# Kernel optimization log

Hardware: AMD Instinct MI355X
Metric: run time of the kernel (lower is better)

## Reference

```python
import jax, jax.numpy as jnp
import numpy as np
import math

HID, HEADS, HD = 1024, 16, 64
DFF = 4 * HID
EPS = 1e-6
RES_SCALE = 0.5

def build_alibi_slopes(n_heads):
    def get_slopes(power):
        start = 2 ** (-2 ** (-(math.log2(power) - 3)))
        return [start * start ** i for i in range(power)]
    if math.log2(n_heads).is_integer():
        slopes = get_slopes(n_heads)
    else:
        closest = 2 ** math.floor(math.log2(n_heads))
        slopes = get_slopes(closest)
        extra = get_slopes(2 * closest)
        slopes = slopes + extra[0::2][: n_heads - closest]
    return jnp.asarray(np.array(slopes, dtype=np.float32))

def rmsnorm(x, w):
    var = jnp.mean(x * x, axis=-1, keepdims=True)
    return x * jax.lax.rsqrt(var + EPS) * w

def setup_inputs() -> dict:
    key = jax.random.key(0)
    ks = jax.random.split(key, 12)
    s = lambda d: 1.0 / math.sqrt(d)
    return {
        "x": jax.random.normal(ks[0], (2, 2048, HID), dtype=jnp.float32),
        "norm1_w": jnp.ones((HID,), jnp.float32),
        "Wq": jax.random.normal(ks[1], (HID, HEADS * HD), jnp.float32) * s(HID),
        "bq": jax.random.normal(ks[2], (HEADS * HD,), jnp.float32) * 0.01,
        "Wk": jax.random.normal(ks[3], (HID, HEADS * HD), jnp.float32) * s(HID),
        "bk": jax.random.normal(ks[4], (HEADS * HD,), jnp.float32) * 0.01,
        "Wv": jax.random.normal(ks[5], (HID, HEADS * HD), jnp.float32) * s(HID),
        "Wo": jax.random.normal(ks[6], (HEADS * HD, HID), jnp.float32) * s(HEADS * HD),
        "norm2_w": jnp.ones((HID,), jnp.float32),
        "W1": jax.random.normal(ks[7], (HID, DFF), jnp.float32) * s(HID),
        "b1": jax.random.normal(ks[8], (DFF,), jnp.float32) * 0.01,
        "W2": jax.random.normal(ks[9], (DFF, HID), jnp.float32) * s(DFF),
        "b2": jax.random.normal(ks[10], (HID,), jnp.float32) * 0.01,
    }

def reference(x, norm1_w, Wq, bq, Wk, bk, Wv, Wo, norm2_w, W1, b1, W2, b2):
    b, s, _ = x.shape
    scale = HD ** -0.5
    xn = rmsnorm(x, norm1_w)
    q = (xn @ Wq + bq).reshape(b, s, HEADS, HD).transpose(0, 2, 1, 3)
    k = (xn @ Wk + bk).reshape(b, s, HEADS, HD).transpose(0, 2, 1, 3)
    v = (xn @ Wv).reshape(b, s, HEADS, HD).transpose(0, 2, 1, 3)
    scores = jnp.einsum('bhqd,bhkd->bhqk', q, k) * scale
    pos = jnp.arange(s)
    dist = jnp.abs(pos[None, :] - pos[:, None]).astype(scores.dtype)  # [s,s]
    slopes = build_alibi_slopes(HEADS)
    bias = -slopes[:, None, None] * dist[None, :, :]  # [h,s,s]
    scores = scores + bias[None]
    weights = jax.nn.softmax(scores, axis=-1)
    attn = jnp.einsum('bhqk,bhkd->bhqd', weights, v)
    attn = attn.transpose(0, 2, 1, 3).reshape(b, s, HEADS * HD)
    x = x + attn @ Wo
    xn2 = rmsnorm(x, norm2_w)
    h = jax.nn.gelu(xn2 @ W1 + b1, approximate=False)
    x = x + RES_SCALE * (h @ W2 + b2)
    return x
```

## Files before the change

kernel.cpp:

```cpp
#include <hip/hip_runtime.h>
#include <hip/hip_bf16.h>
#include <math.h>

#define S_LEN   2048
#define HIDN    1024
#define NHEADS  16
#define HDIM    64
#define NTOK    4096
#define DFFN    4096

#define LOG2E 1.44269504088896f

typedef __attribute__((ext_vector_type(8))) __bf16 bf16x8;
typedef __attribute__((ext_vector_type(4))) float  f32x4;

static __device__ __forceinline__ ushort f2bf(float f) {
  union { float f; unsigned u; } v; v.f = f;
  unsigned u = v.u;
  unsigned r = (u + 0x7fffu + ((u >> 16) & 1u)) >> 16;
  return (ushort)r;
}

#define GLOAD16(gp, lp)                                                              \
  __builtin_amdgcn_global_load_lds((const __attribute__((address_space(1))) void*)(gp), \
                                   (__attribute__((address_space(3))) void*)(lp), 16, 0, 0)

__global__ __launch_bounds__(256) void convert_all(const float* __restrict__ Wq,
                                                   const float* __restrict__ Wk,
                                                   const float* __restrict__ Wv,
                                                   const float* __restrict__ Wo,
                                                   const float* __restrict__ W1,
                                                   const float* __restrict__ W2,
                                                   ushort* __restrict__ wqkvT,
                                                   ushort* __restrict__ woT,
                                                   ushort* __restrict__ w1T,
                                                   ushort* __restrict__ w2T) {
  __shared__ float tile[32][33];
  int id = blockIdx.x;
  const float* W; ushort* WT; int K, N, tl;
  if (id < 3072) {
    int i = id >> 10; tl = id & 1023;
    W = (i == 0) ? Wq : (i == 1) ? Wk : Wv;
    WT = wqkvT + i * 1024 * 1024; K = 1024; N = 1024;
  } else if (id < 4096) { tl = id - 3072; W = Wo; WT = woT; K = 1024; N = 1024; }
  else if (id < 8192)   { tl = id - 4096; W = W1; WT = w1T; K = 1024; N = 4096; }
  else                  { tl = id - 8192; W = W2; WT = w2T; K = 4096; N = 1024; }
  int ntn = N >> 5;
  int n0 = (tl % ntn) * 32, k0 = (tl / ntn) * 32;
  int tx = threadIdx.x & 31, ty = threadIdx.x >> 5;
#pragma unroll
  for (int i = 0; i < 4; i++)
    tile[ty + i * 8][tx] = W[(size_t)(k0 + ty + i * 8) * N + n0 + tx];
  __syncthreads();
#pragma unroll
  for (int i = 0; i < 4; i++)
    WT[(size_t)(n0 + ty + i * 8) * K + k0 + tx] = f2bf(tile[tx][ty + i * 8]);
}

__global__ __launch_bounds__(256) void rmsnorm_kernel(const float* __restrict__ x,
                                                      const float* __restrict__ w,
                                                      ushort* __restrict__ out) {
  int row = blockIdx.x, t = threadIdx.x;
  const float4* x4 = (const float4*)(x + (size_t)row * HIDN);
  float4 v = x4[t];
  float ss = v.x * v.x + v.y * v.y + v.z * v.z + v.w * v.w;
#pragma unroll
  for (int m = 32; m; m >>= 1) ss += __shfl_xor(ss, m, 64);
  __shared__ float wsum[4];
  if ((t & 63) == 0) wsum[t >> 6] = ss;
  __syncthreads();
  float tot = wsum[0] + wsum[1] + wsum[2] + wsum[3];
  float rs = rsqrtf(tot * (1.0f / HIDN) + 1e-6f);
  const float4* w4 = (const float4*)w;
  float4 wv = w4[t];
  ushort4 o;
  o.x = f2bf(v.x * rs * wv.x);
  o.y = f2bf(v.y * rs * wv.y);
  o.z = f2bf(v.z * rs * wv.z);
  o.w = f2bf(v.w * rs * wv.w);
  *(ushort4*)(out + (size_t)row * HIDN + t * 4) = o;
}

template <int EPI, int TM>
__global__ __launch_bounds__(256, 3) void gemm_bt(const ushort* __restrict__ A,
                                                  const ushort* __restrict__ B,
                                                  int M, int N, int K,
                                                  const float* __restrict__ bias,
                                                  const float* __restrict__ resid,
                                                  float* __restrict__ outf,
                                                  ushort* __restrict__ outb,
                                                  ushort* __restrict__ qb,
                                                  ushort* __restrict__ kb,
                                                  ushort* __restrict__ vb) {
  constexpr int NF = (TM == 128) ? 4 : 2;
  __shared__ __align__(16) ushort As[TM * 64];
  __shared__ __align__(16) ushort Bs[128 * 64];
  int t = threadIdx.x;
  int w = t >> 6, l = t & 63;
  int wmr = (TM == 128) ? (w >> 1) * 64 : 0;
  int wnc = (TM == 128) ? (w & 1) * 64 : w * 32;
  int lr = l & 15, lg = l >> 4;

  int nwg = gridDim.x * gridDim.y;
  int bid = blockIdx.y * gridDim.x + blockIdx.x;
  int swz = (bid & 7) * (nwg >> 3) + (bid >> 3);
  int bx = swz % gridDim.x, by = swz / gridDim.x;
  int m0 = bx * TM, n0 = by * 128;

  int srl = l >> 3;
  int sg  = ((l & 7) ^ srl) * 8;
  const ushort* Ag = A + (size_t)(m0 + w * (TM / 4) + srl) * K + sg;
  const ushort* Bg = B + (size_t)(n0 + w * 32 + srl) * K + sg;
  ushort* Asw = &As[(w * (TM / 4)) * 64];
  ushort* Bsw = &Bs[(w * 32) * 64];

  f32x4 acc[4][NF] = {};

  for (int k0 = 0; k0 < K; k0 += 64) {
#pragma unroll
    for (int c = 0; c < TM / 32; c++)
      GLOAD16(Ag + (size_t)(8 * c) * K + k0, Asw + (8 * c) * 64);
#pragma unroll
    for (int c = 0; c < 4; c++)
      GLOAD16(Bg + (size_t)(8 * c) * K + k0, Bsw + (8 * c) * 64);
    __syncthreads();

    bf16x8 af[4][2], bfr[NF][2];
#pragma unroll
    for (int mf = 0; mf < 4; mf++)
#pragma unroll
      for (int ks = 0; ks < 2; ks++)
        af[mf][ks] = *(const bf16x8*)(&As[(wmr + mf * 16 + lr) * 64 +
                                          (((ks * 4 + lg) ^ (lr & 7)) << 3)]);
#pragma unroll
    for (int nf = 0; nf < NF; nf++)
#pragma unroll
      for (int ks = 0; ks < 2; ks++)
        bfr[nf][ks] = *(const bf16x8*)(&Bs[(wnc + nf * 16 + lr) * 64 +
                                           (((ks * 4 + lg) ^ (lr & 7)) << 3)]);
#pragma unroll
    for (int mf = 0; mf < 4; mf++)
#pragma unroll
      for (int nf = 0; nf < NF; nf++) {
        acc[mf][nf] = __builtin_amdgcn_mfma_f32_16x16x32_bf16(af[mf][0], bfr[nf][0], acc[mf][nf], 0, 0, 0);
        acc[mf][nf] = __builtin_amdgcn_mfma_f32_16x16x32_bf16(af[mf][1], bfr[nf][1], acc[mf][nf], 0, 0, 0);
      }
    __syncthreads();
  }

  int lg4 = lg * 4;
  if constexpr (EPI == 0) {
#pragma unroll
    for (int mf = 0; mf < 4; mf++) {
      int row0 = m0 + wmr + mf * 16 + lg4;
      int bb = row0 >> 11, ss0 = row0 & 2047;
#pragma unroll
      for (int nf = 0; nf < NF; nf++) {
        int col = n0 + wnc + nf * 16 + lr;
        int which = col >> 10, nn = col & 1023;
        int hh = nn >> 6, dd = nn & 63;
        float bcol = (which == 0) ? bias[nn] : (which == 1) ? resid[nn] : 0.0f;
        if (which == 2) {
          ushort4 o;
          o.x = f2bf(acc[mf][nf][0]);
          o.y = f2bf(acc[mf][nf][1]);
          o.z = f2bf(acc[mf][nf][2]);
          o.w = f2bf(acc[mf][nf][3]);
          *(ushort4*)(vb + ((size_t)(bb * NHEADS + hh) * HDIM + dd) * S_LEN + ss0) = o;
        } else {
#pragma unroll
          for (int r = 0; r < 4; r++) {
            float v = acc[mf][nf][r] + bcol;
            size_t idx = ((size_t)(bb * NHEADS + hh) * S_LEN + ss0 + r) * HDIM + dd;
            if (which == 0) qb[idx] = f2bf(v * (0.125f * LOG2E));
            else kb[idx] = f2bf(v);
          }
        }
      }
    }
  } else {
#pragma unroll
    for (int mf = 0; mf < 4; mf++) {
#pragma unroll
      for (int nf = 0; nf < NF; nf++) {
#pragma unroll
        for (int r = 0; r < 4; r++) {
          int row = m0 + wmr + mf * 16 + lg4 + r;
          int col = n0 + wnc + nf * 16 + lr;
          float v = acc[mf][nf][r];
          if constexpr (EPI == 1) {
            outf[(size_t)row * HIDN + col] = resid[(size_t)row * HIDN + col] + v;
          } else if constexpr (EPI == 2) {
            float tv = v + bias[col];
            float gl = 0.5f * tv * (1.0f + erff(tv * 0.70710678118f));
            outb[(size_t)row * DFFN + col] = f2bf(gl);
          } else {
            outf[(size_t)row * HIDN + col] =
                resid[(size_t)row * HIDN + col] + 0.5f * (v + bias[col]);
          }
        }
      }
    }
  }
}

__global__ __launch_bounds__(256, 4) void attn_kernel(const ushort* __restrict__ qb,
                                                      const ushort* __restrict__ kb,
                                                      const ushort* __restrict__ vt,
                                                      ushort* __restrict__ attn_out) {
  __shared__ __align__(16) ushort Ks[2][64 * 64];
  __shared__ __align__(16) ushort VTs[2][64 * 64];
  int t = threadIdx.x;
  int w = t >> 6, l = t & 63;
  int lr = l & 15, lg = l >> 4, g8 = lg * 8;

  int nwg = gridDim.x;
  int bid = blockIdx.x;
  int blk = (bid & 7) * (nwg >> 3) + (bid >> 3);
  int qt = blk & 31;
  int bh = blk >> 5;
  int h = bh & 15;
  float slope2 = exp2f(-0.5f * (float)(h + 1)) * LOG2E;
  float s64v = slope2 * 64.0f;
  int q0 = qt * 64;
  const ushort* qp = qb + (size_t)bh * S_LEN * HDIM;
  const ushort* kp = kb + (size_t)bh * S_LEN * HDIM;
  const ushort* vp = vt + (size_t)bh * HDIM * S_LEN;

  int S0 = (l >> 3) & 3;
  size_t kof0 = (size_t)(w * 16 + (l >> 3)) * HDIM + (size_t)(((l & 7) ^ S0) * 8);
  size_t kof1 = (size_t)(w * 16 + 8 + (l >> 3)) * HDIM + (size_t)(((l & 7) ^ S0 ^ 4) * 8);
  size_t vof0 = (size_t)(w * 16 + (l >> 3)) * S_LEN + (size_t)(((l & 7) ^ S0) * 8);
  size_t vof1 = (size_t)(w * 16 + 8 + (l >> 3)) * S_LEN + (size_t)(((l & 7) ^ S0 ^ 4) * 8);

  auto stage = [&](int tile, int b) {
    const ushort* ks_ = kp + (size_t)tile * 64 * HDIM;
    const ushort* vs_ = vp + tile * 64;
    GLOAD16(ks_ + kof0, &Ks[b][(w * 16) * 64]);
    GLOAD16(ks_ + kof1, &Ks[b][(w * 16 + 8) * 64]);
    GLOAD16(vs_ + vof0, &VTs[b][(w * 16) * 64]);
    GLOAD16(vs_ + vof1, &VTs[b][(w * 16 + 8) * 64]);
  };

  bf16x8 qf[2];
#pragma unroll
  for (int ks = 0; ks < 2; ks++)
    qf[ks] = *(const bf16x8*)(qp + (size_t)(q0 + w * 16 + lr) * HDIM + ks * 32 + g8);

  f32x4 ao[4] = {};
  float mrow = -INFINITY, lden = 0.f;

  int qabs = q0 + w * 16 + lr;
  f32x4 biasv[4];
  if (qt > 0) {
#pragma unroll
    for (int nf = 0; nf < 4; nf++)
#pragma unroll
      for (int r = 0; r < 4; r++)
        biasv[nf][r] = -slope2 * (float)(qabs - (32 * (nf >> 1) + 8 * lg + 4 * (nf & 1) + r));
  }

  int kbase_row = ((lr >> 2) << 3) + (lr & 3);
  int SK = (lr & 3) | (((lr >> 2) & 1) << 2);
  int SV = (lr & 3) | (((lr >> 3) & 1) << 2);

  stage(0, 0);
  __syncthreads();

  for (int tt = 0; tt < S_LEN / 64; tt++) {
    int cur = tt & 1;
    if (tt + 1 < S_LEN / 64) stage(tt + 1, cur ^ 1);
    bool diag = (tt == qt);

    f32x4 sc[4];
    __builtin_amdgcn_s_setprio(1);
#pragma unroll
    for (int nf = 0; nf < 4; nf++) {
      int kvr = kbase_row + ((nf & 1) << 2) + ((nf >> 1) << 5);
      f32x4 a = diag ? f32x4{0.f, 0.f, 0.f, 0.f} : biasv[nf];
#pragma unroll
      for (int ks = 0; ks < 2; ks++) {
        bf16x8 kf = *(const bf16x8*)(&Ks[cur][kvr * 64 + (((ks * 4 + lg) ^ SK) << 3)]);
        a = __builtin_amdgcn_mfma_f32_16x16x32_bf16(kf, qf[ks], a, 0, 0, 0);
      }
      sc[nf] = a;
    }
    __builtin_amdgcn_s_setprio(0);

    if (diag) {
      int qq = w * 16 + lr;
#pragma unroll
      for (int nf = 0; nf < 4; nf++)
#pragma unroll
        for (int r = 0; r < 4; r++) {
          int kvloc = 32 * (nf >> 1) + 8 * lg + 4 * (nf & 1) + r;
          sc[nf][r] -= slope2 * fabsf((float)(qq - kvloc));
          biasv[nf][r] = -slope2 * (float)(64 + kvloc - qq);
        }
    }

    float mx = -INFINITY;
#pragma unroll
    for (int nf = 0; nf < 4; nf++)
#pragma unroll
      for (int r = 0; r < 4; r++) mx = fmaxf(mx, sc[nf][r]);
    mx = fmaxf(mx, __shfl_xor(mx, 16, 64));
    mx = fmaxf(mx, __shfl_xor(mx, 32, 64));

    if (__any(mx > mrow)) {
      float mn = fmaxf(mrow, mx);
      float scl = exp2f(mrow - mn);
      mrow = mn;
      lden *= scl;
      float so[4];
#pragma unroll
      for (int r = 0; r < 4; r++) so[r] = __shfl(scl, lg * 4 + r, 64);
#pragma unroll
      for (int nf = 0; nf < 4; nf++)
#pragma unroll
        for (int r = 0; r < 4; r++) ao[nf][r] *= so[r];
    }

    float su = 0.f;
#pragma unroll
    for (int nf = 0; nf < 4; nf++)
#pragma unroll
      for (int r = 0; r < 4; r++) {
        float p = exp2f(sc[nf][r] - mrow);
        sc[nf][r] = p;
        su += p;
      }
    su += __shfl_xor(su, 16, 64);
    su += __shfl_xor(su, 32, 64);
    lden += su;

    bf16x8 pf[2];
#pragma unroll
    for (int ks = 0; ks < 2; ks++)
#pragma unroll
      for (int j = 0; j < 8; j++)
        pf[ks][j] = (__bf16)sc[2 * ks + (j >> 2)][j & 3];

    __builtin_amdgcn_s_setprio(1);
#pragma unroll
    for (int nf = 0; nf < 4; nf++) {
      int d = nf * 16 + lr;
#pragma unroll
      for (int ks = 0; ks < 2; ks++) {
        bf16x8 vf = *(const bf16x8*)(&VTs[cur][d * 64 + (((ks * 4 + lg) ^ SV) << 3)]);
        ao[nf] = __builtin_amdgcn_mfma_f32_16x16x32_bf16(pf[ks], vf, ao[nf], 0, 0, 0);
      }
    }
    __builtin_amdgcn_s_setprio(0);

    int next = tt + 1;
    if (!diag && next != qt) {
      float dd = (next < qt) ? s64v : -s64v;
#pragma unroll
      for (int nf = 0; nf < 4; nf++)
#pragma unroll
        for (int r = 0; r < 4; r++) biasv[nf][r] += dd;
    }
    __syncthreads();
  }

  float inv[4];
#pragma unroll
  for (int r = 0; r < 4; r++) inv[r] = 1.0f / __shfl(lden, lg * 4 + r, 64);
  int token_base = (bh >> 4) * S_LEN + q0 + w * 16;
#pragma unroll
  for (int nf = 0; nf < 4; nf++) {
#pragma unroll
    for (int r = 0; r < 4; r++) {
      int token = token_base + lg * 4 + r;
      int d = nf * 16 + lr;
      attn_out[(size_t)token * HIDN + h * HDIM + d] = f2bf(ao[nf][r] * inv[r]);
    }
  }
}

extern "C" void kernel_launch(void* const* d_in, const int* in_sizes, int n_in,
                              void* d_out, int out_size, void* d_ws, size_t ws_size,
                              hipStream_t stream) {
  const float* x   = (const float*)d_in[0];
  const float* n1w = (const float*)d_in[1];
  const float* Wq  = (const float*)d_in[2];
  const float* bq  = (const float*)d_in[3];
  const float* Wk  = (const float*)d_in[4];
  const float* bk  = (const float*)d_in[5];
  const float* Wv  = (const float*)d_in[6];
  const float* Wo  = (const float*)d_in[7];
  const float* n2w = (const float*)d_in[8];
  const float* W1  = (const float*)d_in[9];
  const float* b1  = (const float*)d_in[10];
  const float* W2  = (const float*)d_in[11];
  const float* b2  = (const float*)d_in[12];
  float* out = (float*)d_out;

  char* ws = (char*)d_ws;
  ushort* xn     = (ushort*)(ws + 0);
  ushort* wqkvT  = (ushort*)(ws + 8388608);
  ushort* woT    = (ushort*)(ws + 14680064);
  ushort* w1T    = (ushort*)(ws + 16777216);
  ushort* w2T    = (ushort*)(ws + 25165824);
  ushort* qbuf   = (ushort*)(ws + 33566720);
  ushort* kbuf   = (ushort*)(ws + 41955328);
  ushort* vtbuf  = (ushort*)(ws + 50343936);
  ushort* attnb  = (ushort*)(ws + 58732544);
  float*  x2     = (float*)(ws + 67121152);
  ushort* xn2    = (ushort*)(ws + 83898368);
  ushort* hbuf   = qbuf;

  dim3 blk(256);

  convert_all<<<dim3(12288), blk, 0, stream>>>(Wq, Wk, Wv, Wo, W1, W2,
                                               wqkvT, woT, w1T, w2T);
  rmsnorm_kernel<<<NTOK, blk, 0, stream>>>(x, n1w, xn);
  gemm_bt<0, 128><<<dim3(32, 24), blk, 0, stream>>>(xn, wqkvT, NTOK, 3 * HIDN, HIDN,
                                                    bq, bk, nullptr, nullptr,
                                                    qbuf, kbuf, vtbuf);
  attn_kernel<<<dim3(32 * 32), blk, 0, stream>>>(qbuf, kbuf, vtbuf, attnb);
  gemm_bt<1, 64><<<dim3(64, 8), blk, 0, stream>>>(attnb, woT, NTOK, HIDN, HIDN,
                                                  nullptr, x, x2, nullptr,
                                                  nullptr, nullptr, nullptr);
  rmsnorm_kernel<<<NTOK, blk, 0, stream>>>(x2, n2w, xn2);
  gemm_bt<2, 128><<<dim3(32, 32), blk, 0, stream>>>(xn2, w1T, NTOK, DFFN, HIDN,
                                                    b1, nullptr, nullptr, hbuf,
                                                    nullptr, nullptr, nullptr);
  gemm_bt<3, 64><<<dim3(64, 8), blk, 0, stream>>>(hbuf, w2T, NTOK, HIDN, DFFN,
                                                  b2, x2, out, nullptr,
                                                  nullptr, nullptr, nullptr);
}
```

Baseline: 382.0 us.

## Split-K the FFN down-projection with atomics, remap attention heads, skip negligible tiles

The final W2 GEMM is split into two K halves across a grid z dimension. Each half adds its partial product into an output that a new elementwise kernel pre-fills with the residual plus the scaled bias. This doubles the workgroup count for a grid that was only 512 blocks, at the cost of float atomics, an extra pass over the output and nondeterministic summation order. Separately, the attention block index mapping is changed to interleave heads with different ALiBi slopes per XCD group, and KV tiles whose row max lies more than 25 (log2 units) below the running max are skipped entirely, dropping exp and PV work for far-away tiles that ALiBi makes negligible.

```diff
diff --git a/kernel.cpp b/kernel.cpp
--- a/kernel.cpp
+++ b/kernel.cpp
@@ -81,17 +81,29 @@
   *(ushort4*)(out + (size_t)row * HIDN + t * 4) = o;
 }
 
+__global__ __launch_bounds__(256) void out_init(const float* __restrict__ x2,
+                                                const float* __restrict__ b2,
+                                                float* __restrict__ out) {
+  int i = blockIdx.x * 256 + threadIdx.x;
+  float4 xv = ((const float4*)x2)[i];
+  float4 bv = ((const float4*)b2)[i & 255];
+  float4 o = {xv.x + 0.5f * bv.x, xv.y + 0.5f * bv.y,
+              xv.z + 0.5f * bv.z, xv.w + 0.5f * bv.w};
+  ((float4*)out)[i] = o;
+}
+
 template <int EPI, int TM>
-__global__ __launch_bounds__(256, 3) void gemm_bt(const ushort* __restrict__ A,
-                                                  const ushort* __restrict__ B,
-                                                  int M, int N, int K,
-                                                  const float* __restrict__ bias,
-                                                  const float* __restrict__ resid,
-                                                  float* __restrict__ outf,
-                                                  ushort* __restrict__ outb,
-                                                  ushort* __restrict__ qb,
-                                                  ushort* __restrict__ kb,
-                                                  ushort* __restrict__ vb) {
+__global__ __launch_bounds__(256, TM == 128 ? 3 : 4)
+void gemm_bt(const ushort* __restrict__ A,
+             const ushort* __restrict__ B,
+             int M, int N, int K,
+             const float* __restrict__ bias,
+             const float* __restrict__ resid,
+             float* __restrict__ outf,
+             ushort* __restrict__ outb,
+             ushort* __restrict__ qb,
+             ushort* __restrict__ kb,
+             ushort* __restrict__ vb) {
   constexpr int NF = (TM == 128) ? 4 : 2;
   __shared__ __align__(16) ushort As[TM * 64];
   __shared__ __align__(16) ushort Bs[128 * 64];
@@ -107,6 +119,9 @@
   int bx = swz % gridDim.x, by = swz / gridDim.x;
   int m0 = bx * TM, n0 = by * 128;
 
+  int klen = (EPI == 5) ? (K >> 1) : K;
+  int kbeg = (EPI == 5) ? blockIdx.z * klen : 0;
+
   int srl = l >> 3;
   int sg  = ((l & 7) ^ srl) * 8;
   const ushort* Ag = A + (size_t)(m0 + w * (TM / 4) + srl) * K + sg;
@@ -116,7 +131,7 @@
 
   f32x4 acc[4][NF] = {};
 
-  for (int k0 = 0; k0 < K; k0 += 64) {
+  for (int k0 = kbeg; k0 < kbeg + klen; k0 += 64) {
 #pragma unroll
     for (int c = 0; c < TM / 32; c++)
       GLOAD16(Ag + (size_t)(8 * c) * K + k0, Asw + (8 * c) * 64);
@@ -194,9 +209,11 @@
             float tv = v + bias[col];
             float gl = 0.5f * tv * (1.0f + erff(tv * 0.70710678118f));
             outb[(size_t)row * DFFN + col] = f2bf(gl);
-          } else {
+          } else if constexpr (EPI == 3) {
             outf[(size_t)row * HIDN + col] =
                 resid[(size_t)row * HIDN + col] + 0.5f * (v + bias[col]);
+          } else {
+            unsafeAtomicAdd(&outf[(size_t)row * HIDN + col], 0.5f * v);
           }
         }
       }
@@ -214,12 +231,12 @@
   int w = t >> 6, l = t & 63;
   int lr = l & 15, lg = l >> 4, g8 = lg * 8;
 
-  int nwg = gridDim.x;
   int bid = blockIdx.x;
-  int blk = (bid & 7) * (nwg >> 3) + (bid >> 3);
-  int qt = blk & 31;
-  int bh = blk >> 5;
-  int h = bh & 15;
+  int v = (bid & 7) * 128 + (bid >> 3);
+  int qt = v & 31;
+  int g = v >> 5;
+  int h = (g >> 1 & 7) + 8 * (g & 1);
+  int bh = (g >> 4) * 16 + h;
   float slope2 = exp2f(-0.5f * (float)(h + 1)) * LOG2E;
   float s64v = slope2 * 64.0f;
   int q0 = qt * 64;
@@ -307,51 +324,53 @@
     mx = fmaxf(mx, __shfl_xor(mx, 16, 64));
     mx = fmaxf(mx, __shfl_xor(mx, 32, 64));
 
-    if (__any(mx > mrow)) {
-      float mn = fmaxf(mrow, mx);
-      float scl = exp2f(mrow - mn);
-      mrow = mn;
-      lden *= scl;
-      float so[4];
-#pragma unroll
-      for (int r = 0; r < 4; r++) so[r] = __shfl(scl, lg * 4 + r, 64);
+    if (!__all(mx < mrow - 25.0f)) {
+      if (__any(mx > mrow)) {
+        float mn = fmaxf(mrow, mx);
+        float scl = exp2f(mrow - mn);
+        mrow = mn;
+        lden *= scl;
+        float so[4];
+#pragma unroll
+        for (int r = 0; r < 4; r++) so[r] = __shfl(scl, lg * 4 + r, 64);
+#pragma unroll
+        for (int nf = 0; nf < 4; nf++)
+#pragma unroll
+          for (int r = 0; r < 4; r++) ao[nf][r] *= so[r];
+      }
+
+      float su = 0.f;
 #pragma unroll
       for (int nf = 0; nf < 4; nf++)
 #pragma unroll
-        for (int r = 0; r < 4; r++) ao[nf][r] *= so[r];
-    }
-
-    float su = 0.f;
-#pragma unroll
-    for (int nf = 0; nf < 4; nf++)
-#pragma unroll
-      for (int r = 0; r < 4; r++) {
-        float p = exp2f(sc[nf][r] - mrow);
-        sc[nf][r] = p;
-        su += p;
-      }
-    su += __shfl_xor(su, 16, 64);
-    su += __shfl_xor(su, 32, 64);
-    lden += su;
-
-    bf16x8 pf[2];
-#pragma unroll
-    for (int ks = 0; ks < 2; ks++)
-#pragma unroll
-      for (int j = 0; j < 8; j++)
-        pf[ks][j] = (__bf16)sc[2 * ks + (j >> 2)][j & 3];
-
-    __builtin_amdgcn_s_setprio(1);
-#pragma unroll
-    for (int nf = 0; nf < 4; nf++) {
-      int d = nf * 16 + lr;
-#pragma unroll
-      for (int ks = 0; ks < 2; ks++) {
-        bf16x8 vf = *(const bf16x8*)(&VTs[cur][d * 64 + (((ks * 4 + lg) ^ SV) << 3)]);
-        ao[nf] = __builtin_amdgcn_mfma_f32_16x16x32_bf16(pf[ks], vf, ao[nf], 0, 0, 0);
-      }
-    }
-    __builtin_amdgcn_s_setprio(0);
+        for (int r = 0; r < 4; r++) {
+          float p = exp2f(sc[nf][r] - mrow);
+          sc[nf][r] = p;
+          su += p;
+        }
+      su += __shfl_xor(su, 16, 64);
+      su += __shfl_xor(su, 32, 64);
+      lden += su;
+
+      bf16x8 pf[2];
+#pragma unroll
+      for (int ks = 0; ks < 2; ks++)
+#pragma unroll
+        for (int j = 0; j < 8; j++)
+          pf[ks][j] = (__bf16)sc[2 * ks + (j >> 2)][j & 3];
+
+      __builtin_amdgcn_s_setprio(1);
+#pragma unroll
+      for (int nf = 0; nf < 4; nf++) {
+        int d = nf * 16 + lr;
+#pragma unroll
+        for (int ks = 0; ks < 2; ks++) {
+          bf16x8 vf = *(const bf16x8*)(&VTs[cur][d * 64 + (((ks * 4 + lg) ^ SV) << 3)]);
+          ao[nf] = __builtin_amdgcn_mfma_f32_16x16x32_bf16(pf[ks], vf, ao[nf], 0, 0, 0);
+        }
+      }
+      __builtin_amdgcn_s_setprio(0);
+    }
 
     int next = tt + 1;
     if (!diag && next != qt) {
@@ -427,7 +446,8 @@
   gemm_bt<2, 128><<<dim3(32, 32), blk, 0, stream>>>(xn2, w1T, NTOK, DFFN, HIDN,
                                                     b1, nullptr, nullptr, hbuf,
                                                     nullptr, nullptr, nullptr);
-  gemm_bt<3, 64><<<dim3(64, 8), blk, 0, stream>>>(hbuf, w2T, NTOK, HIDN, DFFN,
-                                                  b2, x2, out, nullptr,
-                                                  nullptr, nullptr, nullptr);
-}
+  out_init<<<dim3(4096), blk, 0, stream>>>(x2, b2, out);
+  gemm_bt<5, 64><<<dim3(64, 8, 2), blk, 0, stream>>>(hbuf, w2T, NTOK, HIDN, DFFN,
+                                                     nullptr, nullptr, out, nullptr,
+                                                     nullptr, nullptr, nullptr);
+}
```

Measured after the change: 394.4 us. 1.03x slower.
